# Optimization experiments

Hardware: AMD Instinct MI355X
Metric: run time of the kernel (lower is better)

## Reference

```python
import jax, jax.numpy as jnp
import numpy as np

N_EMBD = 1024
N_HEAD = 16

def setup_inputs() -> dict:
    key = jax.random.key(0)
    ks = jax.random.split(key, 5)
    B, T, C = 4, 2048, N_EMBD
    s = 0.02
    return {
        'x': jax.random.normal(ks[0], (B, T, C), jnp.float32),
        'w_attn': jax.random.normal(ks[1], (C, 3 * C), jnp.float32) * s,
        'b_attn': jax.random.normal(ks[2], (3 * C,), jnp.float32) * s,
        'w_proj': jax.random.normal(ks[3], (C, C), jnp.float32) * s,
        'b_proj': jax.random.normal(ks[4], (C,), jnp.float32) * s,
    }

def reference(x, w_attn, b_attn, w_proj, b_proj):
    B, T, C = x.shape
    H = N_HEAD
    D = C // H  # head dim
    qkv = x @ w_attn + b_attn                      # [B,T,3C]
    q, k, v = jnp.split(qkv, 3, axis=-1)
    q = q.reshape(B, T, H, D).transpose(0, 2, 1, 3)  # [B,H,T,D]
    k = k.reshape(B, T, H, D).transpose(0, 2, 1, 3)
    v = v.reshape(B, T, H, D).transpose(0, 2, 1, 3)
    att = jnp.einsum('bhqd,bhkd->bhqk', q, k) * (1.0 / jnp.sqrt(jnp.float32(D)))
    causal = jnp.tril(jnp.ones((T, T), bool))
    att = jnp.where(causal[None, None], att, jnp.float32(-jnp.inf))
    att = jax.nn.softmax(att, axis=-1)
    y = jnp.einsum('bhqk,bhkd->bhqd', att, v)      # [B,H,T,D]
    y = y.transpose(0, 2, 1, 3).reshape(B, T, C)
    return y @ w_proj + b_proj
```

## Files before the change

kernel.cpp:

```cpp
#include <hip/hip_runtime.h>
#include <math.h>

typedef short s16x8 __attribute__((ext_vector_type(8)));
typedef unsigned short u16;
typedef unsigned short u16x4 __attribute__((ext_vector_type(4)));
typedef float f32x4 __attribute__((ext_vector_type(4)));

__device__ __forceinline__ f32x4 mfma16(s16x8 a, s16x8 b, f32x4 c) {
  return __builtin_amdgcn_mfma_f32_16x16x32_bf16(a, b, c, 0, 0, 0);
}

__device__ __forceinline__ u16 f2bf(float f) {
  unsigned u = __builtin_bit_cast(unsigned, f);
  u = (u + 0x7fffu + ((u >> 16) & 1u)) >> 16;
  return (u16)u;
}

__device__ __forceinline__ unsigned pk_trunc(float hi, float lo) {
  return __builtin_amdgcn_perm(__builtin_bit_cast(unsigned, hi),
                               __builtin_bit_cast(unsigned, lo), 0x07060302u);
}

__device__ __forceinline__ void gll16(const void* g, void* l) {
  __builtin_amdgcn_global_load_lds((__attribute__((address_space(1))) void*)(void*)g,
                                   (__attribute__((address_space(3))) void*)l,
                                   16, 0, 0);
}

__device__ __forceinline__ void lds_fence() {
  asm volatile("s_waitcnt lgkmcnt(0)" ::: "memory");
}

__global__ __launch_bounds__(256) void k_convert_x(const float* __restrict__ x,
                                                   u16* __restrict__ xb) {
  int i = (blockIdx.x * 256 + threadIdx.x) * 8;
  const float4* xv = (const float4*)(x + i);
  float4 a = xv[0], b = xv[1];
  union { s16x8 v; u16 s[8]; } r;
  r.s[0] = f2bf(a.x); r.s[1] = f2bf(a.y); r.s[2] = f2bf(a.z); r.s[3] = f2bf(a.w);
  r.s[4] = f2bf(b.x); r.s[5] = f2bf(b.y); r.s[6] = f2bf(b.z); r.s[7] = f2bf(b.w);
  *(s16x8*)(xb + i) = r.v;
}

__global__ __launch_bounds__(256) void k_transpose_w(const float* __restrict__ in,
                                                     u16* __restrict__ out, int R, int C) {
  __shared__ float tile[32][33];
  int c0 = blockIdx.x * 32, r0 = blockIdx.y * 32;
  int tx = threadIdx.x & 31, ty = threadIdx.x >> 5;
#pragma unroll
  for (int s = 0; s < 4; ++s)
    tile[ty + 8 * s][tx] = in[(size_t)(r0 + ty + 8 * s) * C + c0 + tx];
  __syncthreads();
#pragma unroll
  for (int s = 0; s < 4; ++s)
    out[(size_t)(c0 + ty + 8 * s) * R + r0 + tx] = f2bf(tile[tx][ty + 8 * s]);
}

__global__ __launch_bounds__(256) void k_transpose_v(const u16* __restrict__ v,
                                                     u16* __restrict__ vt) {
  __shared__ u16 tile[64][65];
  int bh = blockIdx.y, t0 = blockIdx.x * 64, tid = threadIdx.x;
#pragma unroll
  for (int p = 0; p < 16; ++p) {
    int idx = p * 256 + tid;
    int tt = idx >> 6, dd = idx & 63;
    tile[dd][tt] = v[((size_t)bh * 2048 + t0 + tt) * 64 + dd];
  }
  __syncthreads();
#pragma unroll
  for (int p = 0; p < 16; ++p) {
    int idx = p * 256 + tid;
    int dd = idx >> 6, tt = idx & 63;
    vt[((size_t)bh * 64 + dd) * 2048 + t0 + tt] = tile[dd][tt];
  }
}

template <int EPI>
__global__ __launch_bounds__(256) void k_gemm(const u16* __restrict__ A,
                                              const u16* __restrict__ Bt,
                                              const float* __restrict__ bias,
                                              float* __restrict__ outp,
                                              u16* __restrict__ q_out,
                                              u16* __restrict__ k_out,
                                              u16* __restrict__ v_out,
                                              int K, int nIter) {
  __shared__ u16 As[4096];
  __shared__ u16 Bs[4096];
  int tid = threadIdx.x, w = tid >> 6, l = tid & 63;
  int r = l & 15, qd = l >> 4;
  int id = blockIdx.x;
  int xcd = id & 7, s0 = id >> 3;
  int mBlk = xcd * 8 + (s0 & 7);
  int nBlk = s0 >> 3;
  f32x4 acc[4][4] = {};

  const u16* ga[2]; const u16* gb[2]; u16* la[2]; u16* lb[2];
#pragma unroll
  for (int qq = 0; qq < 2; ++qq) {
    int grp = 2 * w + qq;
    int rowA = mBlk * 128 + grp * 16 + (l >> 2);
    int rowB = nBlk * 128 + grp * 16 + (l >> 2);
    int kcol = (l & 3) * 8;
    ga[qq] = A + (size_t)rowA * K + kcol;
    gb[qq] = Bt + (size_t)rowB * K + kcol;
    la[qq] = As + grp * 512;
    lb[qq] = Bs + grp * 512;
  }
  int aoff = ((w & 1) * 4) * 512 + r * 32 + qd * 8;
  int boff = ((w >> 1) * 4) * 512 + r * 32 + qd * 8;

  for (int kt = 0; kt < nIter; ++kt) {
#pragma unroll
    for (int qq = 0; qq < 2; ++qq) { gll16(ga[qq], la[qq]); gll16(gb[qq], lb[qq]); }
    ga[0] += 32; ga[1] += 32; gb[0] += 32; gb[1] += 32;
    __syncthreads();
    s16x8 af[4], bf[4];
#pragma unroll
    for (int i = 0; i < 4; ++i) af[i] = *(const s16x8*)(As + aoff + i * 512);
#pragma unroll
    for (int j = 0; j < 4; ++j) bf[j] = *(const s16x8*)(Bs + boff + j * 512);
#pragma unroll
    for (int i = 0; i < 4; ++i)
#pragma unroll
      for (int j = 0; j < 4; ++j) acc[i][j] = mfma16(af[i], bf[j], acc[i][j]);
    __syncthreads();
  }

  const float QSCALE = 0.125f * 1.44269504088896f;
  int rowBase = mBlk * 128 + (w & 1) * 64;
  int colBase = nBlk * 128 + (w >> 1) * 64;
#pragma unroll
  for (int i = 0; i < 4; ++i) {
#pragma unroll
    for (int j = 0; j < 4; ++j) {
      int col = colBase + j * 16 + r;
      float bv = bias[col];
#pragma unroll
      for (int g = 0; g < 4; ++g) {
        int row = rowBase + i * 16 + qd * 4 + g;
        float v = acc[i][j][g] + bv;
        if (EPI == 0) {
          int which = col >> 10;
          int rem = col & 1023;
          int hh = rem >> 6, dd = rem & 63;
          int bb = row >> 11, tt = row & 2047;
          u16* base = (which == 0) ? q_out : (which == 1) ? k_out : v_out;
          if (which == 0) v *= QSCALE;
          base[(((size_t)(bb * 16 + hh)) * 2048 + tt) * 64 + dd] = f2bf(v);
        } else {
          outp[(size_t)row * 1024 + col] = v;
        }
      }
    }
  }
}

__global__ __launch_bounds__(256) void k_attn(const u16* __restrict__ qg,
                                              const u16* __restrict__ kg,
                                              const u16* __restrict__ vtg,
                                              u16* __restrict__ yg) {
  __shared__ u16 Ks[2][64 * 64];
  __shared__ u16 Vs[2][64 * 64];
  __shared__ u16 Ps[4][16 * 64];

  int bh = blockIdx.y, bb = bh >> 4, hh = bh & 15;
  int bx = blockIdx.x;
  int tid = threadIdx.x, w = tid >> 6, l = tid & 63;
  int r = l & 15, qd = l >> 4;
  int psw = (r & 7) * 8;

  int chunkA = bx, chunkB = 31 - bx;
  int nA = bx + 1, nB = 32 - bx;
  int qloc = w * 16 + r;

  s16x8 qf[2][2];
#pragma unroll
  for (int i = 0; i < 2; ++i) {
    int qbase = (i == 0 ? chunkA : chunkB) * 64 + w * 16;
#pragma unroll
    for (int s = 0; s < 2; ++s)
      qf[i][s] = *(const s16x8*)(qg + ((size_t)bh * 2048 + qbase + r) * 64 + s * 32 + qd * 8);
  }

  s16x8 onesf;
#pragma unroll
  for (int e = 0; e < 8; ++e) onesf[e] = (short)0x3F80;

  f32x4 o[2][4] = {};
  f32x4 lacc[2] = {};

  int rl = l >> 3;
  int cg = (l & 7) ^ rl;
  const u16* kbase = kg + (size_t)bh * 2048 * 64;
  const u16* vbase = vtg + (size_t)bh * 64 * 2048;

  auto stage = [&](int kt, int buf) {
    int kk0 = kt * 64;
#pragma unroll
    for (int p = 0; p < 2; ++p) {
      int row = p * 32 + w * 8 + rl;
      gll16(kbase + ((size_t)(kk0 + row)) * 64 + cg * 8, Ks[buf] + p * 2048 + w * 512);
      gll16(vbase + (size_t)row * 2048 + kk0 + cg * 8, Vs[buf] + p * 2048 + w * 512);
    }
  };

  stage(0, 0);
  __syncthreads();

  for (int kt = 0; kt < nB; ++kt) {
    int cur = kt & 1;
    if (kt + 1 < nB) stage(kt + 1, cur ^ 1);

    bool doA = (kt < nA);
    f32x4 sacc[2][4] = {};
#pragma unroll
    for (int s = 0; s < 2; ++s) {
#pragma unroll
      for (int j = 0; j < 4; ++j) {
        s16x8 kf = *(const s16x8*)(Ks[cur] + (16 * j + r) * 64 + ((s * 4 + qd) ^ (r & 7)) * 8);
        if (doA) sacc[0][j] = mfma16(kf, qf[0][s], sacc[0][j]);
        sacc[1][j] = mfma16(kf, qf[1][s], sacc[1][j]);
      }
    }

#pragma unroll
    for (int i = 0; i < 2; ++i) {
      if (i == 0 && !doA) continue;
      bool needMask = (kt == (i == 0 ? chunkA : chunkB));
      if (i == 1) lds_fence();
#pragma unroll
      for (int j = 0; j < 4; ++j) {
        float p0, p1, p2, p3;
        if (needMask) {
          int kb0 = 16 * j + 4 * qd;
          p0 = (kb0 + 0 > qloc) ? 0.f : __builtin_amdgcn_exp2f(sacc[i][j][0]);
          p1 = (kb0 + 1 > qloc) ? 0.f : __builtin_amdgcn_exp2f(sacc[i][j][1]);
          p2 = (kb0 + 2 > qloc) ? 0.f : __builtin_amdgcn_exp2f(sacc[i][j][2]);
          p3 = (kb0 + 3 > qloc) ? 0.f : __builtin_amdgcn_exp2f(sacc[i][j][3]);
        } else {
          p0 = __builtin_amdgcn_exp2f(sacc[i][j][0]);
          p1 = __builtin_amdgcn_exp2f(sacc[i][j][1]);
          p2 = __builtin_amdgcn_exp2f(sacc[i][j][2]);
          p3 = __builtin_amdgcn_exp2f(sacc[i][j][3]);
        }
        uint2 pk;
        pk.x = pk_trunc(p1, p0);
        pk.y = pk_trunc(p3, p2);
        *(uint2*)(Ps[w] + r * 64 + ((j * 16 + qd * 4) ^ psw)) = pk;
      }
      lds_fence();

#pragma unroll
      for (int s = 0; s < 2; ++s) {
        s16x8 pa = *(const s16x8*)(Ps[w] + r * 64 + ((s * 32 + qd * 8) ^ psw));
        lacc[i] = mfma16(onesf, pa, lacc[i]);
#pragma unroll
        for (int j = 0; j < 4; ++j) {
          s16x8 vf = *(const s16x8*)(Vs[cur] + (16 * j + r) * 64 + ((s * 4 + qd) ^ (r & 7)) * 8);
          o[i][j] = mfma16(vf, pa, o[i][j]);
        }
      }
    }
    __syncthreads();
  }

#pragma unroll
  for (int i = 0; i < 2; ++i) {
    int qbase = (i == 0 ? chunkA : chunkB) * 64 + w * 16;
    float inv = 1.0f / lacc[i][0];
    size_t rowoff = ((size_t)bb * 2048 + qbase + r) * 1024 + hh * 64;
#pragma unroll
    for (int j = 0; j < 4; ++j) {
      u16x4 yv;
      yv[0] = f2bf(o[i][j][0] * inv);
      yv[1] = f2bf(o[i][j][1] * inv);
      yv[2] = f2bf(o[i][j][2] * inv);
      yv[3] = f2bf(o[i][j][3] * inv);
      *(u16x4*)(yg + rowoff + 16 * j + 4 * qd) = yv;
    }
  }
}

extern "C" void kernel_launch(void* const* d_in, const int* in_sizes, int n_in,
                              void* d_out, int out_size, void* d_ws, size_t ws_size,
                              hipStream_t stream) {
  const float* x      = (const float*)d_in[0];
  const float* w_attn = (const float*)d_in[1];
  const float* b_attn = (const float*)d_in[2];
  const float* w_proj = (const float*)d_in[3];
  const float* b_proj = (const float*)d_in[4];
  float* out = (float*)d_out;

  char* ws = (char*)d_ws;
  size_t off = 0;
  auto alloc = [&](size_t bytes) -> void* {
    void* p = ws + off;
    off += (bytes + 255) & ~(size_t)255;
    return p;
  };
  const size_t BT = 8192, C = 1024;
  u16* xb  = (u16*)alloc(BT * C * 2);
  u16* waT = (u16*)alloc(3072 * 1024 * 2);
  u16* wpT = (u16*)alloc(1024 * 1024 * 2);
  u16* qb  = (u16*)alloc(BT * C * 2);
  u16* kb  = (u16*)alloc(BT * C * 2);
  u16* vb  = (u16*)alloc(BT * C * 2);
  u16* vtb = (u16*)alloc(BT * C * 2);
  (void)ws_size; (void)in_sizes; (void)n_in; (void)out_size;

  k_convert_x<<<4096, 256, 0, stream>>>(x, xb);
  k_transpose_w<<<dim3(96, 32), 256, 0, stream>>>(w_attn, waT, 1024, 3072);
  k_transpose_w<<<dim3(32, 32), 256, 0, stream>>>(w_proj, wpT, 1024, 1024);
  k_gemm<0><<<1536, 256, 0, stream>>>(xb, waT, b_attn, nullptr, qb, kb, vb, 1024, 32);
  k_transpose_v<<<dim3(32, 64), 256, 0, stream>>>(vb, vtb);
  k_attn<<<dim3(16, 64), 256, 0, stream>>>(qb, kb, vtb, xb );
  k_gemm<1><<<512, 256, 0, stream>>>(xb, wpT, b_proj, out, nullptr, nullptr, nullptr, 1024, 32);
}
```

Before: 296.9 us.

## Fuse V transpose into QKV GEMM epilogue; process four query chunks per attention block

The QKV GEMM epilogue now writes V directly in transposed [bh][d][t] layout with 4-wide packed stores, which removes the separate V transpose kernel and its intermediate buffer. The attention kernel now handles four causally balanced query chunks per block instead of two, so each staged K/V tile is reused by four chunk-wide MFMA groups, and the grid is halved. This raises register and LDS pressure (larger P buffer, four sets of accumulators), and launch_bounds requests 2 blocks per CU. With 512 blocks, occupancy may be lower on a 256-CU device.

```diff
diff --git a/kernel.cpp b/kernel.cpp
--- a/kernel.cpp
+++ b/kernel.cpp
@@ -56,25 +56,6 @@
     out[(size_t)(c0 + ty + 8 * s) * R + r0 + tx] = f2bf(tile[tx][ty + 8 * s]);
 }
 
-__global__ __launch_bounds__(256) void k_transpose_v(const u16* __restrict__ v,
-                                                     u16* __restrict__ vt) {
-  __shared__ u16 tile[64][65];
-  int bh = blockIdx.y, t0 = blockIdx.x * 64, tid = threadIdx.x;
-#pragma unroll
-  for (int p = 0; p < 16; ++p) {
-    int idx = p * 256 + tid;
-    int tt = idx >> 6, dd = idx & 63;
-    tile[dd][tt] = v[((size_t)bh * 2048 + t0 + tt) * 64 + dd];
-  }
-  __syncthreads();
-#pragma unroll
-  for (int p = 0; p < 16; ++p) {
-    int idx = p * 256 + tid;
-    int dd = idx >> 6, tt = idx & 63;
-    vt[((size_t)bh * 64 + dd) * 2048 + t0 + tt] = tile[dd][tt];
-  }
-}
-
 template <int EPI>
 __global__ __launch_bounds__(256) void k_gemm(const u16* __restrict__ A,
                                               const u16* __restrict__ Bt,
@@ -82,7 +63,7 @@
                                               float* __restrict__ outp,
                                               u16* __restrict__ q_out,
                                               u16* __restrict__ k_out,
-                                              u16* __restrict__ v_out,
+                                              u16* __restrict__ vt_out,
                                               int K, int nIter) {
   __shared__ u16 As[4096];
   __shared__ u16 Bs[4096];
@@ -135,33 +116,45 @@
     for (int j = 0; j < 4; ++j) {
       int col = colBase + j * 16 + r;
       float bv = bias[col];
-#pragma unroll
-      for (int g = 0; g < 4; ++g) {
-        int row = rowBase + i * 16 + qd * 4 + g;
-        float v = acc[i][j][g] + bv;
-        if (EPI == 0) {
-          int which = col >> 10;
-          int rem = col & 1023;
-          int hh = rem >> 6, dd = rem & 63;
-          int bb = row >> 11, tt = row & 2047;
-          u16* base = (which == 0) ? q_out : (which == 1) ? k_out : v_out;
-          if (which == 0) v *= QSCALE;
-          base[(((size_t)(bb * 16 + hh)) * 2048 + tt) * 64 + dd] = f2bf(v);
+      float vv[4];
+#pragma unroll
+      for (int g = 0; g < 4; ++g) vv[g] = acc[i][j][g] + bv;
+      int row0 = rowBase + i * 16 + qd * 4;
+      if (EPI == 0) {
+        int which = col >> 10;
+        int rem = col & 1023;
+        int hh = rem >> 6, dd = rem & 63;
+        int bb = row0 >> 11, tt0 = row0 & 2047;
+        if (which == 2) {
+          u16x4 pk;
+#pragma unroll
+          for (int g = 0; g < 4; ++g) pk[g] = f2bf(vv[g]);
+          *(u16x4*)(vt_out + (((size_t)(bb * 16 + hh)) * 64 + dd) * 2048 + tt0) = pk;
         } else {
-          outp[(size_t)row * 1024 + col] = v;
+          u16* base = (which == 0) ? q_out : k_out;
+#pragma unroll
+          for (int g = 0; g < 4; ++g) {
+            float v = vv[g];
+            if (which == 0) v *= QSCALE;
+            base[(((size_t)(bb * 16 + hh)) * 2048 + tt0 + g) * 64 + dd] = f2bf(v);
+          }
         }
+      } else {
+#pragma unroll
+        for (int g = 0; g < 4; ++g)
+          outp[(size_t)(row0 + g) * 1024 + col] = vv[g];
       }
     }
   }
 }
 
-__global__ __launch_bounds__(256) void k_attn(const u16* __restrict__ qg,
-                                              const u16* __restrict__ kg,
-                                              const u16* __restrict__ vtg,
-                                              u16* __restrict__ yg) {
+__global__ __launch_bounds__(256, 2) void k_attn(const u16* __restrict__ qg,
+                                                 const u16* __restrict__ kg,
+                                                 const u16* __restrict__ vtg,
+                                                 u16* __restrict__ yg) {
   __shared__ u16 Ks[2][64 * 64];
   __shared__ u16 Vs[2][64 * 64];
-  __shared__ u16 Ps[4][16 * 64];
+  __shared__ u16 Ps[4][64 * 64];
 
   int bh = blockIdx.y, bb = bh >> 4, hh = bh & 15;
   int bx = blockIdx.x;
@@ -169,25 +162,26 @@
   int r = l & 15, qd = l >> 4;
   int psw = (r & 7) * 8;
 
-  int chunkA = bx, chunkB = 31 - bx;
-  int nA = bx + 1, nB = 32 - bx;
+  const int chunk[4] = {bx, 15 - bx, 16 + bx, 31 - bx};
+  const int nend[4]  = {bx + 1, 16 - bx, 17 + bx, 32 - bx};
+  int nmax = 32 - bx;
   int qloc = w * 16 + r;
 
-  s16x8 qf[2][2];
-#pragma unroll
-  for (int i = 0; i < 2; ++i) {
-    int qbase = (i == 0 ? chunkA : chunkB) * 64 + w * 16;
+  s16x8 qf[4][2];
+#pragma unroll
+  for (int c = 0; c < 4; ++c) {
+    int qbase = chunk[c] * 64 + w * 16;
 #pragma unroll
     for (int s = 0; s < 2; ++s)
-      qf[i][s] = *(const s16x8*)(qg + ((size_t)bh * 2048 + qbase + r) * 64 + s * 32 + qd * 8);
+      qf[c][s] = *(const s16x8*)(qg + ((size_t)bh * 2048 + qbase + r) * 64 + s * 32 + qd * 8);
   }
 
   s16x8 onesf;
 #pragma unroll
   for (int e = 0; e < 8; ++e) onesf[e] = (short)0x3F80;
 
-  f32x4 o[2][4] = {};
-  f32x4 lacc[2] = {};
+  f32x4 o[4][4] = {};
+  f32x4 lacc[4] = {};
 
   int rl = l >> 3;
   int cg = (l & 7) ^ rl;
@@ -207,75 +201,86 @@
   stage(0, 0);
   __syncthreads();
 
-  for (int kt = 0; kt < nB; ++kt) {
+  for (int kt = 0; kt < nmax; ++kt) {
     int cur = kt & 1;
-    if (kt + 1 < nB) stage(kt + 1, cur ^ 1);
-
-    bool doA = (kt < nA);
-    f32x4 sacc[2][4] = {};
+    if (kt + 1 < nmax) stage(kt + 1, cur ^ 1);
+
+    f32x4 sacc[4][4];
+#pragma unroll
+    for (int c = 0; c < 4; ++c)
+      if (kt < nend[c])
+#pragma unroll
+        for (int j = 0; j < 4; ++j) sacc[c][j] = f32x4{0.f, 0.f, 0.f, 0.f};
 #pragma unroll
     for (int s = 0; s < 2; ++s) {
 #pragma unroll
       for (int j = 0; j < 4; ++j) {
         s16x8 kf = *(const s16x8*)(Ks[cur] + (16 * j + r) * 64 + ((s * 4 + qd) ^ (r & 7)) * 8);
-        if (doA) sacc[0][j] = mfma16(kf, qf[0][s], sacc[0][j]);
-        sacc[1][j] = mfma16(kf, qf[1][s], sacc[1][j]);
+#pragma unroll
+        for (int c = 0; c < 4; ++c)
+          if (kt < nend[c]) sacc[c][j] = mfma16(kf, qf[c][s], sacc[c][j]);
       }
     }
 
 #pragma unroll
-    for (int i = 0; i < 2; ++i) {
-      if (i == 0 && !doA) continue;
-      bool needMask = (kt == (i == 0 ? chunkA : chunkB));
-      if (i == 1) lds_fence();
+    for (int c = 0; c < 4; ++c) {
+      if (kt >= nend[c]) continue;
+      bool needMask = (kt == chunk[c]);
 #pragma unroll
       for (int j = 0; j < 4; ++j) {
         float p0, p1, p2, p3;
         if (needMask) {
           int kb0 = 16 * j + 4 * qd;
-          p0 = (kb0 + 0 > qloc) ? 0.f : __builtin_amdgcn_exp2f(sacc[i][j][0]);
-          p1 = (kb0 + 1 > qloc) ? 0.f : __builtin_amdgcn_exp2f(sacc[i][j][1]);
-          p2 = (kb0 + 2 > qloc) ? 0.f : __builtin_amdgcn_exp2f(sacc[i][j][2]);
-          p3 = (kb0 + 3 > qloc) ? 0.f : __builtin_amdgcn_exp2f(sacc[i][j][3]);
+          p0 = (kb0 + 0 > qloc) ? 0.f : __builtin_amdgcn_exp2f(sacc[c][j][0]);
+          p1 = (kb0 + 1 > qloc) ? 0.f : __builtin_amdgcn_exp2f(sacc[c][j][1]);
+          p2 = (kb0 + 2 > qloc) ? 0.f : __builtin_amdgcn_exp2f(sacc[c][j][2]);
+          p3 = (kb0 + 3 > qloc) ? 0.f : __builtin_amdgcn_exp2f(sacc[c][j][3]);
         } else {
-          p0 = __builtin_amdgcn_exp2f(sacc[i][j][0]);
-          p1 = __builtin_amdgcn_exp2f(sacc[i][j][1]);
-          p2 = __builtin_amdgcn_exp2f(sacc[i][j][2]);
-          p3 = __builtin_amdgcn_exp2f(sacc[i][j][3]);
+          p0 = __builtin_amdgcn_exp2f(sacc[c][j][0]);
+          p1 = __builtin_amdgcn_exp2f(sacc[c][j][1]);
+          p2 = __builtin_amdgcn_exp2f(sacc[c][j][2]);
+          p3 = __builtin_amdgcn_exp2f(sacc[c][j][3]);
         }
         uint2 pk;
         pk.x = pk_trunc(p1, p0);
         pk.y = pk_trunc(p3, p2);
-        *(uint2*)(Ps[w] + r * 64 + ((j * 16 + qd * 4) ^ psw)) = pk;
+        *(uint2*)(Ps[w] + (c * 16 + r) * 64 + ((j * 16 + qd * 4) ^ psw)) = pk;
       }
-      lds_fence();
-
-#pragma unroll
-      for (int s = 0; s < 2; ++s) {
-        s16x8 pa = *(const s16x8*)(Ps[w] + r * 64 + ((s * 32 + qd * 8) ^ psw));
-        lacc[i] = mfma16(onesf, pa, lacc[i]);
-#pragma unroll
-        for (int j = 0; j < 4; ++j) {
-          s16x8 vf = *(const s16x8*)(Vs[cur] + (16 * j + r) * 64 + ((s * 4 + qd) ^ (r & 7)) * 8);
-          o[i][j] = mfma16(vf, pa, o[i][j]);
+    }
+    lds_fence();
+
+#pragma unroll
+    for (int s = 0; s < 2; ++s) {
+      s16x8 pa[4];
+#pragma unroll
+      for (int c = 0; c < 4; ++c)
+        if (kt < nend[c]) {
+          pa[c] = *(const s16x8*)(Ps[w] + (c * 16 + r) * 64 + ((s * 32 + qd * 8) ^ psw));
+          lacc[c] = mfma16(onesf, pa[c], lacc[c]);
         }
+#pragma unroll
+      for (int j = 0; j < 4; ++j) {
+        s16x8 vf = *(const s16x8*)(Vs[cur] + (16 * j + r) * 64 + ((s * 4 + qd) ^ (r & 7)) * 8);
+#pragma unroll
+        for (int c = 0; c < 4; ++c)
+          if (kt < nend[c]) o[c][j] = mfma16(vf, pa[c], o[c][j]);
       }
     }
     __syncthreads();
   }
 
 #pragma unroll
-  for (int i = 0; i < 2; ++i) {
-    int qbase = (i == 0 ? chunkA : chunkB) * 64 + w * 16;
-    float inv = 1.0f / lacc[i][0];
+  for (int c = 0; c < 4; ++c) {
+    int qbase = chunk[c] * 64 + w * 16;
+    float inv = 1.0f / lacc[c][0];
     size_t rowoff = ((size_t)bb * 2048 + qbase + r) * 1024 + hh * 64;
 #pragma unroll
     for (int j = 0; j < 4; ++j) {
       u16x4 yv;
-      yv[0] = f2bf(o[i][j][0] * inv);
-      yv[1] = f2bf(o[i][j][1] * inv);
-      yv[2] = f2bf(o[i][j][2] * inv);
-      yv[3] = f2bf(o[i][j][3] * inv);
+      yv[0] = f2bf(o[c][j][0] * inv);
+      yv[1] = f2bf(o[c][j][1] * inv);
+      yv[2] = f2bf(o[c][j][2] * inv);
+      yv[3] = f2bf(o[c][j][3] * inv);
       *(u16x4*)(yg + rowoff + 16 * j + 4 * qd) = yv;
     }
   }
@@ -304,15 +309,13 @@
   u16* wpT = (u16*)alloc(1024 * 1024 * 2);
   u16* qb  = (u16*)alloc(BT * C * 2);
   u16* kb  = (u16*)alloc(BT * C * 2);
-  u16* vb  = (u16*)alloc(BT * C * 2);
   u16* vtb = (u16*)alloc(BT * C * 2);
   (void)ws_size; (void)in_sizes; (void)n_in; (void)out_size;
 
   k_convert_x<<<4096, 256, 0, stream>>>(x, xb);
   k_transpose_w<<<dim3(96, 32), 256, 0, stream>>>(w_attn, waT, 1024, 3072);
   k_transpose_w<<<dim3(32, 32), 256, 0, stream>>>(w_proj, wpT, 1024, 1024);
-  k_gemm<0><<<1536, 256, 0, stream>>>(xb, waT, b_attn, nullptr, qb, kb, vb, 1024, 32);
-  k_transpose_v<<<dim3(32, 64), 256, 0, stream>>>(vb, vtb);
-  k_attn<<<dim3(16, 64), 256, 0, stream>>>(qb, kb, vtb, xb );
+  k_gemm<0><<<1536, 256, 0, stream>>>(xb, waT, b_attn, nullptr, qb, kb, vtb, 1024, 32);
+  k_attn<<<dim3(8, 64), 256, 0, stream>>>(qb, kb, vtb, xb );
   k_gemm<1><<<512, 256, 0, stream>>>(xb, wpT, b_proj, out, nullptr, nullptr, nullptr, 1024, 32);
 }
```

Measured after the change: 277.9 us. 6.4% less time.
